# Kernel tuning notes

Hardware: AMD Instinct MI355X
Metric: run time of the kernel (lower is better)

## Reference

```python
import jax, jax.numpy as jnp
import numpy as np

B, T, D, K = 256, 256, 768, 128  # batch, seq_len, num_dims, num_state


def setup_inputs() -> dict:
    key = jax.random.key(0)
    k1, k2, k3 = jax.random.split(key, 3)
    s = jax.random.normal(k1, (B, T, D), dtype=jnp.float32)          # embeddings
    means = jax.random.normal(k2, (K, D), dtype=jnp.float32)         # per-state Gaussian means
    var = jax.random.uniform(k3, (D,), dtype=jnp.float32,
                             minval=0.5, maxval=1.5)                  # shared diagonal variance
    return {"s": s, "means": means, "var": var}


def reference(s, means, var):
    """DMVFlow._eval_log_density: per-state diagonal-Gaussian log density.

    density[b,t,k] = -0.5*(D*log(2*pi) + sum_d log var[d])
                     -0.5*sum_d (s[b,t,d] - means[k,d])^2 / var[d]
    Expanded quadratic form so the k-contraction is a single GEMM instead of
    materializing a (B,T,K,D) broadcast.
    """
    d = s.shape[-1]
    inv_var = 1.0 / var                                              # (D,)
    log_norm = -0.5 * (d * jnp.log(2.0 * jnp.pi) + jnp.sum(jnp.log(var)))
    s2 = jnp.einsum('btd,d->bt', s * s, inv_var)                     # (B,T)
    cross = jnp.einsum('btd,kd->btk', s, means * inv_var)            # (B,T,K) GEMM
    m2 = jnp.einsum('kd,d->k', means * means, inv_var)               # (K,)
    quad = s2[..., None] - 2.0 * cross + m2                          # (B,T,K)
    return log_norm - 0.5 * quad
```

## Files before the change

### kernel.cpp

```cpp
#include <hip/hip_runtime.h>
#include <stdint.h>

#define D_DIM    768
#define K_STATES 128
#define M_ROWS   65536
#define BM       64
#define BK       32
#define NSTEPS   (D_DIM / BK)
#define LDSTRIDE 40

typedef __attribute__((ext_vector_type(8))) short bf16x8;
typedef __attribute__((ext_vector_type(4))) float f32x4;
typedef __attribute__((ext_vector_type(4))) int   i32x4;

__device__ __forceinline__ unsigned short f2bf(float f) {
    union { float f; unsigned u; } x; x.f = f;
    unsigned r = (x.u + 0x7FFFu + ((x.u >> 16) & 1u)) >> 16;
    return (unsigned short)r;
}

__global__ void __launch_bounds__(256) prep_kernel(
        const float* __restrict__ means, const float* __restrict__ var,
        unsigned short* __restrict__ mwbf, float* __restrict__ cvec) {
    const int k = blockIdx.x;
    const int t = threadIdx.x;
    float m2 = 0.f, ld = 0.f;
    for (int d = t; d < D_DIM; d += 256) {
        float v  = var[d];
        float iv = 1.0f / v;
        float m  = means[k * D_DIM + d];
        mwbf[k * D_DIM + d] = f2bf(m * iv);
        m2 += m * m * iv;
        ld += logf(v);
    }
#pragma unroll
    for (int off = 32; off > 0; off >>= 1) {
        m2 += __shfl_down(m2, off, 64);
        ld += __shfl_down(ld, off, 64);
    }
    __shared__ float rm[4], rl[4];
    const int wid = t >> 6;
    if ((t & 63) == 0) { rm[wid] = m2; rl[wid] = ld; }
    __syncthreads();
    if (t == 0) {
        float M2 = rm[0] + rm[1] + rm[2] + rm[3];
        float LD = rl[0] + rl[1] + rl[2] + rl[3];
        cvec[k] = -0.5f * ((float)D_DIM * 1.8378770664093453f + LD + M2);
    }
}

__global__ void __launch_bounds__(256, 4) dmv_main(
        const float* __restrict__ s, const unsigned short* __restrict__ mwbf,
        const float* __restrict__ var, const float* __restrict__ cvec,
        float* __restrict__ out) {
    __shared__ unsigned short As[2][BM * LDSTRIDE];
    __shared__ unsigned short Bs[2][K_STATES * LDSTRIDE];
    __shared__ float ivs[D_DIM];
    __shared__ float part[BM][8];
    __shared__ float s2row[BM];
    __shared__ float cs[K_STATES];

    const int t    = threadIdx.x;
    const int lane = t & 63;
    const int w    = t >> 6;
    const int wr   = w >> 1;
    const int wc   = w & 1;
    const long rowBase = (long)blockIdx.x * BM;

    for (int d = t; d < D_DIM; d += 256) ivs[d] = 1.0f / var[d];
    if (t < K_STATES) cs[t] = cvec[t];

    const int arow0 = t >> 3;
    const int acol  = (t & 7) * 4;
    const int brow0 = t >> 2;
    const int bcol  = (t & 3) * 8;

    const float*          sA = s    + (rowBase + arow0) * D_DIM + acol;
    const unsigned short* sB = mwbf + brow0 * D_DIM + bcol;

    f32x4 aPref[2];
    i32x4 bPref[2];
    float s2acc[2] = {0.f, 0.f};

    f32x4 acc[2][4];
#pragma unroll
    for (int i = 0; i < 2; ++i)
#pragma unroll
        for (int j = 0; j < 4; ++j) acc[i][j] = f32x4{0.f, 0.f, 0.f, 0.f};

    auto stageWrite = [&](int buf, int k0) {
        f32x4 ivv = *reinterpret_cast<const f32x4*>(&ivs[k0 + acol]);
#pragma unroll
        for (int j = 0; j < 2; ++j) {
            const int row = j * 32 + arow0;
            f32x4 v = aPref[j];
            s2acc[j] += v[0]*v[0]*ivv[0] + v[1]*v[1]*ivv[1]
                      + v[2]*v[2]*ivv[2] + v[3]*v[3]*ivv[3];
            unsigned u0 = (unsigned)f2bf(v[0]) | ((unsigned)f2bf(v[1]) << 16);
            unsigned u1 = (unsigned)f2bf(v[2]) | ((unsigned)f2bf(v[3]) << 16);
            *reinterpret_cast<uint2*>(&As[buf][row * LDSTRIDE + acol]) = make_uint2(u0, u1);
        }
#pragma unroll
        for (int j = 0; j < 2; ++j) {
            const int row = j * 64 + brow0;
            *reinterpret_cast<i32x4*>(&Bs[buf][row * LDSTRIDE + bcol]) = bPref[j];
        }
    };

#pragma unroll
    for (int j = 0; j < 2; ++j) aPref[j] = *(const f32x4*)(sA + (long)j * 32 * D_DIM);
#pragma unroll
    for (int j = 0; j < 2; ++j) bPref[j] = *(const i32x4*)(sB + j * 64 * D_DIM);
    __syncthreads();
    stageWrite(0, 0);

    const int g  = (lane >> 4) * 8;
    const int rA = wr * 32 + (lane & 15);
    const int rB = wc * 64 + (lane & 15);

    for (int st = 0; st < NSTEPS; ++st) {
        const int cur = st & 1;
        const int k0n = (st + 1) * BK;
        if (st + 1 < NSTEPS) {
#pragma unroll
            for (int j = 0; j < 2; ++j)
                aPref[j] = *(const f32x4*)(sA + (long)j * 32 * D_DIM + k0n);
#pragma unroll
            for (int j = 0; j < 2; ++j)
                bPref[j] = *(const i32x4*)(sB + j * 64 * D_DIM + k0n);
        }
        __syncthreads();

        const unsigned short* Ab = &As[cur][0];
        const unsigned short* Bb = &Bs[cur][0];
        bf16x8 afrag[2], bfrag[4];
#pragma unroll
        for (int i = 0; i < 2; ++i)
            afrag[i] = *(const bf16x8*)(Ab + (rA + i * 16) * LDSTRIDE + g);
#pragma unroll
        for (int j = 0; j < 4; ++j)
            bfrag[j] = *(const bf16x8*)(Bb + (rB + j * 16) * LDSTRIDE + g);
#pragma unroll
        for (int i = 0; i < 2; ++i)
#pragma unroll
            for (int j = 0; j < 4; ++j)
                acc[i][j] = __builtin_amdgcn_mfma_f32_16x16x32_bf16(
                                afrag[i], bfrag[j], acc[i][j], 0, 0, 0);

        if (st + 1 < NSTEPS) stageWrite((st + 1) & 1, k0n);
    }

#pragma unroll
    for (int j = 0; j < 2; ++j) part[j * 32 + arow0][t & 7] = s2acc[j];
    __syncthreads();
    if (t < BM) {
        float v = 0.f;
#pragma unroll
        for (int sl = 0; sl < 8; ++sl) v += part[t][sl];
        s2row[t] = v;
    }
    __syncthreads();

    const int colBase = wc * 64 + (lane & 15);
#pragma unroll
    for (int i = 0; i < 2; ++i) {
        const int rl0 = wr * 32 + i * 16 + (lane >> 4) * 4;
#pragma unroll
        for (int j = 0; j < 4; ++j) {
            const int col = colBase + j * 16;
            const float cj = cs[col];
#pragma unroll
            for (int r = 0; r < 4; ++r) {
                const int rl = rl0 + r;
                out[(rowBase + rl) * K_STATES + col] = acc[i][j][r] + cj - 0.5f * s2row[rl];
            }
        }
    }
}

extern "C" void kernel_launch(void* const* d_in, const int* in_sizes, int n_in,
                              void* d_out, int out_size, void* d_ws, size_t ws_size,
                              hipStream_t stream) {
    const float* s     = (const float*)d_in[0];
    const float* means = (const float*)d_in[1];
    const float* var   = (const float*)d_in[2];
    float* out = (float*)d_out;

    unsigned short* mwbf = (unsigned short*)d_ws;
    float* cvec = (float*)((char*)d_ws + (size_t)K_STATES * D_DIM * sizeof(unsigned short));

    prep_kernel<<<K_STATES, 256, 0, stream>>>(means, var, mwbf, cvec);
    dmv_main<<<M_ROWS / BM, 256, 0, stream>>>(s, mwbf, var, cvec, out);
}
```

Before: 45.02 us.

## Fuse means/var preprocessing into main GEMM kernel and use nontemporal loads/stores

Removes the separate prep kernel. Each block of the main kernel now loads fp32 means directly, scales them by inverse variance, converts them to bf16 in LDS, and computes the per-state m2 and log-variance constants itself. The goal is to save one kernel launch and the workspace round trip. In exchange, every one of the 1024 blocks redoes the means scaling and bf16 conversion and fetches twice the B bytes (fp32 instead of bf16). The streaming s loads and output stores are also marked nontemporal, and the launch_bounds occupancy hint is dropped.

```diff
diff --git a/kernel.cpp b/kernel.cpp
--- a/kernel.cpp
+++ b/kernel.cpp
@@ -19,46 +19,16 @@
     return (unsigned short)r;
 }
 
-__global__ void __launch_bounds__(256) prep_kernel(
-        const float* __restrict__ means, const float* __restrict__ var,
-        unsigned short* __restrict__ mwbf, float* __restrict__ cvec) {
-    const int k = blockIdx.x;
-    const int t = threadIdx.x;
-    float m2 = 0.f, ld = 0.f;
-    for (int d = t; d < D_DIM; d += 256) {
-        float v  = var[d];
-        float iv = 1.0f / v;
-        float m  = means[k * D_DIM + d];
-        mwbf[k * D_DIM + d] = f2bf(m * iv);
-        m2 += m * m * iv;
-        ld += logf(v);
-    }
-#pragma unroll
-    for (int off = 32; off > 0; off >>= 1) {
-        m2 += __shfl_down(m2, off, 64);
-        ld += __shfl_down(ld, off, 64);
-    }
-    __shared__ float rm[4], rl[4];
-    const int wid = t >> 6;
-    if ((t & 63) == 0) { rm[wid] = m2; rl[wid] = ld; }
-    __syncthreads();
-    if (t == 0) {
-        float M2 = rm[0] + rm[1] + rm[2] + rm[3];
-        float LD = rl[0] + rl[1] + rl[2] + rl[3];
-        cvec[k] = -0.5f * ((float)D_DIM * 1.8378770664093453f + LD + M2);
-    }
-}
-
-__global__ void __launch_bounds__(256, 4) dmv_main(
-        const float* __restrict__ s, const unsigned short* __restrict__ mwbf,
-        const float* __restrict__ var, const float* __restrict__ cvec,
-        float* __restrict__ out) {
+__global__ void __launch_bounds__(256) dmv_fused(
+        const float* __restrict__ s, const float* __restrict__ means,
+        const float* __restrict__ var, float* __restrict__ out) {
     __shared__ unsigned short As[2][BM * LDSTRIDE];
     __shared__ unsigned short Bs[2][K_STATES * LDSTRIDE];
     __shared__ float ivs[D_DIM];
     __shared__ float part[BM][8];
     __shared__ float s2row[BM];
     __shared__ float cs[K_STATES];
+    __shared__ float rlg[4];
 
     const int t    = threadIdx.x;
     const int lane = t & 63;
@@ -67,20 +37,28 @@
     const int wc   = w & 1;
     const long rowBase = (long)blockIdx.x * BM;
 
-    for (int d = t; d < D_DIM; d += 256) ivs[d] = 1.0f / var[d];
-    if (t < K_STATES) cs[t] = cvec[t];
+    float ldp = 0.f;
+    for (int d = t; d < D_DIM; d += 256) {
+        float v = var[d];
+        ivs[d] = 1.0f / v;
+        ldp += logf(v);
+    }
+#pragma unroll
+    for (int off = 32; off > 0; off >>= 1) ldp += __shfl_down(ldp, off, 64);
+    if ((t & 63) == 0) rlg[t >> 6] = ldp;
 
     const int arow0 = t >> 3;
     const int acol  = (t & 7) * 4;
-    const int brow0 = t >> 2;
-    const int bcol  = (t & 3) * 8;
+    const int brow  = t >> 1;
+    const int bcol0 = (t & 1) * 16;
 
-    const float*          sA = s    + (rowBase + arow0) * D_DIM + acol;
-    const unsigned short* sB = mwbf + brow0 * D_DIM + bcol;
+    const float* sA = s     + (rowBase + arow0) * D_DIM + acol;
+    const float* sM = means + brow * D_DIM + bcol0;
 
     f32x4 aPref[2];
-    i32x4 bPref[2];
+    f32x4 bPref[4];
     float s2acc[2] = {0.f, 0.f};
+    float m2p = 0.f;
 
     f32x4 acc[2][4];
 #pragma unroll
@@ -100,18 +78,36 @@
             unsigned u1 = (unsigned)f2bf(v[2]) | ((unsigned)f2bf(v[3]) << 16);
             *reinterpret_cast<uint2*>(&As[buf][row * LDSTRIDE + acol]) = make_uint2(u0, u1);
         }
+        f32x4 mw[4];
 #pragma unroll
-        for (int j = 0; j < 2; ++j) {
-            const int row = j * 64 + brow0;
-            *reinterpret_cast<i32x4*>(&Bs[buf][row * LDSTRIDE + bcol]) = bPref[j];
+        for (int j = 0; j < 4; ++j) {
+            f32x4 iw = *reinterpret_cast<const f32x4*>(&ivs[k0 + bcol0 + j * 4]);
+            f32x4 mv = bPref[j];
+            m2p += mv[0]*mv[0]*iw[0] + mv[1]*mv[1]*iw[1]
+                 + mv[2]*mv[2]*iw[2] + mv[3]*mv[3]*iw[3];
+            mw[j] = f32x4{mv[0]*iw[0], mv[1]*iw[1], mv[2]*iw[2], mv[3]*iw[3]};
         }
+        i32x4 p0, p1;
+        p0.x = (int)((unsigned)f2bf(mw[0][0]) | ((unsigned)f2bf(mw[0][1]) << 16));
+        p0.y = (int)((unsigned)f2bf(mw[0][2]) | ((unsigned)f2bf(mw[0][3]) << 16));
+        p0.z = (int)((unsigned)f2bf(mw[1][0]) | ((unsigned)f2bf(mw[1][1]) << 16));
+        p0.w = (int)((unsigned)f2bf(mw[1][2]) | ((unsigned)f2bf(mw[1][3]) << 16));
+        p1.x = (int)((unsigned)f2bf(mw[2][0]) | ((unsigned)f2bf(mw[2][1]) << 16));
+        p1.y = (int)((unsigned)f2bf(mw[2][2]) | ((unsigned)f2bf(mw[2][3]) << 16));
+        p1.z = (int)((unsigned)f2bf(mw[3][0]) | ((unsigned)f2bf(mw[3][1]) << 16));
+        p1.w = (int)((unsigned)f2bf(mw[3][2]) | ((unsigned)f2bf(mw[3][3]) << 16));
+        *reinterpret_cast<i32x4*>(&Bs[buf][brow * LDSTRIDE + bcol0])     = p0;
+        *reinterpret_cast<i32x4*>(&Bs[buf][brow * LDSTRIDE + bcol0 + 8]) = p1;
     };
 
 #pragma unroll
-    for (int j = 0; j < 2; ++j) aPref[j] = *(const f32x4*)(sA + (long)j * 32 * D_DIM);
+    for (int j = 0; j < 2; ++j)
+        aPref[j] = __builtin_nontemporal_load((const f32x4*)(sA + (long)j * 32 * D_DIM));
 #pragma unroll
-    for (int j = 0; j < 2; ++j) bPref[j] = *(const i32x4*)(sB + j * 64 * D_DIM);
+    for (int j = 0; j < 4; ++j)
+        bPref[j] = *(const f32x4*)(sM + j * 4);
     __syncthreads();
+    const float slog = rlg[0] + rlg[1] + rlg[2] + rlg[3];
     stageWrite(0, 0);
 
     const int g  = (lane >> 4) * 8;
@@ -124,10 +120,11 @@
         if (st + 1 < NSTEPS) {
 #pragma unroll
             for (int j = 0; j < 2; ++j)
-                aPref[j] = *(const f32x4*)(sA + (long)j * 32 * D_DIM + k0n);
+                aPref[j] = __builtin_nontemporal_load(
+                               (const f32x4*)(sA + (long)j * 32 * D_DIM + k0n));
 #pragma unroll
-            for (int j = 0; j < 2; ++j)
-                bPref[j] = *(const i32x4*)(sB + j * 64 * D_DIM + k0n);
+            for (int j = 0; j < 4; ++j)
+                bPref[j] = *(const f32x4*)(sM + k0n + j * 4);
         }
         __syncthreads();
 
@@ -152,6 +149,11 @@
 
 #pragma unroll
     for (int j = 0; j < 2; ++j) part[j * 32 + arow0][t & 7] = s2acc[j];
+    {
+        float m2t = m2p + __shfl_xor(m2p, 1, 64);
+        if (!(t & 1))
+            cs[brow] = -0.5f * ((float)D_DIM * 1.8378770664093453f + slog + m2t);
+    }
     __syncthreads();
     if (t < BM) {
         float v = 0.f;
@@ -172,7 +174,8 @@
 #pragma unroll
             for (int r = 0; r < 4; ++r) {
                 const int rl = rl0 + r;
-                out[(rowBase + rl) * K_STATES + col] = acc[i][j][r] + cj - 0.5f * s2row[rl];
+                __builtin_nontemporal_store(acc[i][j][r] + cj - 0.5f * s2row[rl],
+                                            &out[(rowBase + rl) * K_STATES + col]);
             }
         }
     }
@@ -186,9 +189,5 @@
     const float* var   = (const float*)d_in[2];
     float* out = (float*)d_out;
 
-    unsigned short* mwbf = (unsigned short*)d_ws;
-    float* cvec = (float*)((char*)d_ws + (size_t)K_STATES * D_DIM * sizeof(unsigned short));
-
-    prep_kernel<<<K_STATES, 256, 0, stream>>>(means, var, mwbf, cvec);
-    dmv_main<<<M_ROWS / BM, 256, 0, stream>>>(s, mwbf, var, cvec, out);
+    dmv_fused<<<M_ROWS / BM, 256, 0, stream>>>(s, means, var, out);
 }
```

New measurement: 77.87 us. +73.0%, slower.

## Load GEMM operands directly into MFMA fragments, dropping LDS staging

Applied to the files above, without the earlier changes.

Removes the shared-memory double buffering of A and B tiles. Each wave now loads its own 32 rows of s and all 128 rows of the bf16 means straight from global memory into registers laid out as MFMA fragments, with a two-stage register prefetch. The block tile doubles to 128 rows and each wave holds all 128 output columns. The per-row s2 reduction now uses cross-lane shuffles instead of LDS, and outputs use nontemporal stores. The aim is to cut LDS traffic and barriers, at the cost of many more registers, lower occupancy, and every wave re-reading the B matrix from global memory or cache.

```diff
diff --git a/kernel.cpp b/kernel.cpp
--- a/kernel.cpp
+++ b/kernel.cpp
@@ -4,10 +4,9 @@
 #define D_DIM    768
 #define K_STATES 128
 #define M_ROWS   65536
-#define BM       64
+#define BM       128
 #define BK       32
 #define NSTEPS   (D_DIM / BK)
-#define LDSTRIDE 40
 
 typedef __attribute__((ext_vector_type(8))) short bf16x8;
 typedef __attribute__((ext_vector_type(4))) float f32x4;
@@ -49,133 +48,114 @@
     }
 }
 
-__global__ void __launch_bounds__(256, 4) dmv_main(
+__global__ void __launch_bounds__(256, 2) dmv_main(
         const float* __restrict__ s, const unsigned short* __restrict__ mwbf,
         const float* __restrict__ var, const float* __restrict__ cvec,
         float* __restrict__ out) {
-    __shared__ unsigned short As[2][BM * LDSTRIDE];
-    __shared__ unsigned short Bs[2][K_STATES * LDSTRIDE];
     __shared__ float ivs[D_DIM];
-    __shared__ float part[BM][8];
-    __shared__ float s2row[BM];
-    __shared__ float cs[K_STATES];
 
     const int t    = threadIdx.x;
     const int lane = t & 63;
     const int w    = t >> 6;
-    const int wr   = w >> 1;
-    const int wc   = w & 1;
-    const long rowBase = (long)blockIdx.x * BM;
+    const int r0   = lane & 15;
+    const int g    = (lane >> 4) * 8;
+    const long rowBase = (long)blockIdx.x * BM + w * 32;
 
-    for (int d = t; d < D_DIM; d += 256) ivs[d] = 1.0f / var[d];
-    if (t < K_STATES) cs[t] = cvec[t];
+    const float*          pA = s    + (rowBase + r0) * D_DIM + g;
+    const unsigned short* pB = mwbf + r0 * D_DIM + g;
 
-    const int arow0 = t >> 3;
-    const int acol  = (t & 7) * 4;
-    const int brow0 = t >> 2;
-    const int bcol  = (t & 3) * 8;
-
-    const float*          sA = s    + (rowBase + arow0) * D_DIM + acol;
-    const unsigned short* sB = mwbf + brow0 * D_DIM + bcol;
-
-    f32x4 aPref[2];
-    i32x4 bPref[2];
-    float s2acc[2] = {0.f, 0.f};
-
-    f32x4 acc[2][4];
+    f32x4 acc[2][8];
 #pragma unroll
     for (int i = 0; i < 2; ++i)
 #pragma unroll
-        for (int j = 0; j < 4; ++j) acc[i][j] = f32x4{0.f, 0.f, 0.f, 0.f};
+        for (int j = 0; j < 8; ++j) acc[i][j] = f32x4{0.f, 0.f, 0.f, 0.f};
 
-    auto stageWrite = [&](int buf, int k0) {
-        f32x4 ivv = *reinterpret_cast<const f32x4*>(&ivs[k0 + acol]);
-#pragma unroll
-        for (int j = 0; j < 2; ++j) {
-            const int row = j * 32 + arow0;
-            f32x4 v = aPref[j];
-            s2acc[j] += v[0]*v[0]*ivv[0] + v[1]*v[1]*ivv[1]
-                      + v[2]*v[2]*ivv[2] + v[3]*v[3]*ivv[3];
-            unsigned u0 = (unsigned)f2bf(v[0]) | ((unsigned)f2bf(v[1]) << 16);
-            unsigned u1 = (unsigned)f2bf(v[2]) | ((unsigned)f2bf(v[3]) << 16);
-            *reinterpret_cast<uint2*>(&As[buf][row * LDSTRIDE + acol]) = make_uint2(u0, u1);
-        }
-#pragma unroll
-        for (int j = 0; j < 2; ++j) {
-            const int row = j * 64 + brow0;
-            *reinterpret_cast<i32x4*>(&Bs[buf][row * LDSTRIDE + bcol]) = bPref[j];
-        }
-    };
+    f32x4 a0_[2][2], a1_[2][2];
+    i32x4 b0_[8], b1_[8];
 
-#pragma unroll
-    for (int j = 0; j < 2; ++j) aPref[j] = *(const f32x4*)(sA + (long)j * 32 * D_DIM);
-#pragma unroll
-    for (int j = 0; j < 2; ++j) bPref[j] = *(const i32x4*)(sB + j * 64 * D_DIM);
+#define LOADA(DST, ST) do {                                                    \
+    _Pragma("unroll")                                                          \
+    for (int i = 0; i < 2; ++i) {                                              \
+        const float* p = pA + (long)i * 16 * D_DIM + (ST) * BK;                \
+        DST[i][0] = *(const f32x4*)(p);                                        \
+        DST[i][1] = *(const f32x4*)(p + 4);                                    \
+    } } while (0)
+
+#define LOADB(DST, ST) do {                                                    \
+    _Pragma("unroll")                                                          \
+    for (int j = 0; j < 8; ++j)                                                \
+        DST[j] = *(const i32x4*)(pB + (long)j * 16 * D_DIM + (ST) * BK);       \
+    } while (0)
+
+    LOADA(a0_, 0); LOADB(b0_, 0);
+    LOADA(a1_, 1); LOADB(b1_, 1);
+
+    for (int d = t; d < D_DIM; d += 256) ivs[d] = 1.0f / var[d];
     __syncthreads();
-    stageWrite(0, 0);
 
-    const int g  = (lane >> 4) * 8;
-    const int rA = wr * 32 + (lane & 15);
-    const int rB = wc * 64 + (lane & 15);
+    float s2acc[2] = {0.f, 0.f};
 
-    for (int st = 0; st < NSTEPS; ++st) {
-        const int cur = st & 1;
-        const int k0n = (st + 1) * BK;
-        if (st + 1 < NSTEPS) {
-#pragma unroll
-            for (int j = 0; j < 2; ++j)
-                aPref[j] = *(const f32x4*)(sA + (long)j * 32 * D_DIM + k0n);
-#pragma unroll
-            for (int j = 0; j < 2; ++j)
-                bPref[j] = *(const i32x4*)(sB + j * 64 * D_DIM + k0n);
-        }
-        __syncthreads();
+#define STEP(ARAW, BRAW, K0) do {                                              \
+    f32x4 iv0 = *(const f32x4*)&ivs[(K0) + g];                                 \
+    f32x4 iv1 = *(const f32x4*)&ivs[(K0) + g + 4];                             \
+    bf16x8 af[2];                                                              \
+    _Pragma("unroll")                                                          \
+    for (int i = 0; i < 2; ++i) {                                              \
+        f32x4 v0 = ARAW[i][0], v1 = ARAW[i][1];                                \
+        s2acc[i] += v0[0]*v0[0]*iv0[0] + v0[1]*v0[1]*iv0[1]                    \
+                  + v0[2]*v0[2]*iv0[2] + v0[3]*v0[3]*iv0[3]                    \
+                  + v1[0]*v1[0]*iv1[0] + v1[1]*v1[1]*iv1[1]                    \
+                  + v1[2]*v1[2]*iv1[2] + v1[3]*v1[3]*iv1[3];                   \
+        union { bf16x8 h; unsigned u[4]; } pk;                                 \
+        pk.u[0] = (unsigned)f2bf(v0[0]) | ((unsigned)f2bf(v0[1]) << 16);       \
+        pk.u[1] = (unsigned)f2bf(v0[2]) | ((unsigned)f2bf(v0[3]) << 16);       \
+        pk.u[2] = (unsigned)f2bf(v1[0]) | ((unsigned)f2bf(v1[1]) << 16);       \
+        pk.u[3] = (unsigned)f2bf(v1[2]) | ((unsigned)f2bf(v1[3]) << 16);       \
+        af[i] = pk.h;                                                          \
+    }                                                                          \
+    _Pragma("unroll")                                                          \
+    for (int j = 0; j < 8; ++j) {                                              \
+        union { i32x4 i; bf16x8 h; } bb; bb.i = BRAW[j];                       \
+        acc[0][j] = __builtin_amdgcn_mfma_f32_16x16x32_bf16(af[0], bb.h,       \
+                                                            acc[0][j], 0,0,0);\
+        acc[1][j] = __builtin_amdgcn_mfma_f32_16x16x32_bf16(af[1], bb.h,       \
+                                                            acc[1][j], 0,0,0);\
+    } } while (0)
 
-        const unsigned short* Ab = &As[cur][0];
-        const unsigned short* Bb = &Bs[cur][0];
-        bf16x8 afrag[2], bfrag[4];
-#pragma unroll
-        for (int i = 0; i < 2; ++i)
-            afrag[i] = *(const bf16x8*)(Ab + (rA + i * 16) * LDSTRIDE + g);
-#pragma unroll
-        for (int j = 0; j < 4; ++j)
-            bfrag[j] = *(const bf16x8*)(Bb + (rB + j * 16) * LDSTRIDE + g);
-#pragma unroll
-        for (int i = 0; i < 2; ++i)
-#pragma unroll
-            for (int j = 0; j < 4; ++j)
-                acc[i][j] = __builtin_amdgcn_mfma_f32_16x16x32_bf16(
-                                afrag[i], bfrag[j], acc[i][j], 0, 0, 0);
-
-        if (st + 1 < NSTEPS) stageWrite((st + 1) & 1, k0n);
+    for (int st = 0; st < NSTEPS; st += 2) {
+        STEP(a0_, b0_, st * BK);
+        if (st + 2 < NSTEPS) { LOADA(a0_, st + 2); LOADB(b0_, st + 2); }
+        STEP(a1_, b1_, (st + 1) * BK);
+        if (st + 3 < NSTEPS) { LOADA(a1_, st + 3); LOADB(b1_, st + 3); }
     }
 
 #pragma unroll
-    for (int j = 0; j < 2; ++j) part[j * 32 + arow0][t & 7] = s2acc[j];
-    __syncthreads();
-    if (t < BM) {
-        float v = 0.f;
+    for (int i = 0; i < 2; ++i) {
+        s2acc[i] += __shfl_xor(s2acc[i], 16, 64);
+        s2acc[i] += __shfl_xor(s2acc[i], 32, 64);
+    }
+
+    float cj[8];
 #pragma unroll
-        for (int sl = 0; sl < 8; ++sl) v += part[t][sl];
-        s2row[t] = v;
-    }
-    __syncthreads();
+    for (int j = 0; j < 8; ++j) cj[j] = cvec[j * 16 + r0];
 
-    const int colBase = wc * 64 + (lane & 15);
+    const int q = lane >> 4;
 #pragma unroll
     for (int i = 0; i < 2; ++i) {
-        const int rl0 = wr * 32 + i * 16 + (lane >> 4) * 4;
 #pragma unroll
-        for (int j = 0; j < 4; ++j) {
-            const int col = colBase + j * 16;
-            const float cj = cs[col];
+        for (int r = 0; r < 4; ++r) {
+            float s2v = __shfl(s2acc[i], q * 4 + r, 64);
+            const long row = rowBase + i * 16 + q * 4 + r;
+            float* po = out + row * K_STATES + r0;
+            const float base = -0.5f * s2v;
 #pragma unroll
-            for (int r = 0; r < 4; ++r) {
-                const int rl = rl0 + r;
-                out[(rowBase + rl) * K_STATES + col] = acc[i][j][r] + cj - 0.5f * s2row[rl];
-            }
+            for (int j = 0; j < 8; ++j)
+                __builtin_nontemporal_store(acc[i][j][r] + cj[j] + base, po + j * 16);
         }
     }
+#undef LOADA
+#undef LOADB
+#undef STEP
 }
 
 extern "C" void kernel_launch(void* const* d_in, const int* in_sizes, int n_in,
```

Result: slower. 79.23 us (+76.0%).

## Deepen global prefetch to two register stages and unroll K loop by two

Applied to the files above, without the earlier changes.

Holds two register prefetch sets so global loads for step st+2/st+3 are issued two iterations ahead, and unrolls the K loop by two with fixed LDS buffer indices. It also swaps the manual bf16 rounding for the HIP __float22bfloat162_rn packed conversion. The aim is to hide more global-memory latency and cut index and select overhead. In exchange it uses more registers, which could hurt the 4-blocks-per-CU occupancy target.

```diff
diff --git a/kernel.cpp b/kernel.cpp
--- a/kernel.cpp
+++ b/kernel.cpp
@@ -1,4 +1,5 @@
 #include <hip/hip_runtime.h>
+#include <hip/hip_bf16.h>
 #include <stdint.h>
 
 #define D_DIM    768
@@ -78,8 +79,8 @@
     const float*          sA = s    + (rowBase + arow0) * D_DIM + acol;
     const unsigned short* sB = mwbf + brow0 * D_DIM + bcol;
 
-    f32x4 aPref[2];
-    i32x4 bPref[2];
+    f32x4 a0_[2], a1_[2];
+    i32x4 b0_[2], b1_[2];
     float s2acc[2] = {0.f, 0.f};
 
     f32x4 acc[2][4];
@@ -88,66 +89,72 @@
 #pragma unroll
         for (int j = 0; j < 4; ++j) acc[i][j] = f32x4{0.f, 0.f, 0.f, 0.f};
 
-    auto stageWrite = [&](int buf, int k0) {
-        f32x4 ivv = *reinterpret_cast<const f32x4*>(&ivs[k0 + acol]);
-#pragma unroll
-        for (int j = 0; j < 2; ++j) {
-            const int row = j * 32 + arow0;
-            f32x4 v = aPref[j];
-            s2acc[j] += v[0]*v[0]*ivv[0] + v[1]*v[1]*ivv[1]
-                      + v[2]*v[2]*ivv[2] + v[3]*v[3]*ivv[3];
-            unsigned u0 = (unsigned)f2bf(v[0]) | ((unsigned)f2bf(v[1]) << 16);
-            unsigned u1 = (unsigned)f2bf(v[2]) | ((unsigned)f2bf(v[3]) << 16);
-            *reinterpret_cast<uint2*>(&As[buf][row * LDSTRIDE + acol]) = make_uint2(u0, u1);
-        }
-#pragma unroll
-        for (int j = 0; j < 2; ++j) {
-            const int row = j * 64 + brow0;
-            *reinterpret_cast<i32x4*>(&Bs[buf][row * LDSTRIDE + bcol]) = bPref[j];
-        }
-    };
-
-#pragma unroll
-    for (int j = 0; j < 2; ++j) aPref[j] = *(const f32x4*)(sA + (long)j * 32 * D_DIM);
-#pragma unroll
-    for (int j = 0; j < 2; ++j) bPref[j] = *(const i32x4*)(sB + j * 64 * D_DIM);
-    __syncthreads();
-    stageWrite(0, 0);
+#define LOADP(AP, BP, ST) do {                                                 \
+    AP[0] = *(const f32x4*)(sA + (ST) * BK);                                   \
+    AP[1] = *(const f32x4*)(sA + (long)32 * D_DIM + (ST) * BK);                \
+    BP[0] = *(const i32x4*)(sB + (ST) * BK);                                   \
+    BP[1] = *(const i32x4*)(sB + (long)64 * D_DIM + (ST) * BK);                \
+} while (0)
+
+#define STAGE(BUF, AP, BP, K0) do {                                            \
+    f32x4 ivv = *reinterpret_cast<const f32x4*>(&ivs[(K0) + acol]);            \
+    _Pragma("unroll")                                                          \
+    for (int j = 0; j < 2; ++j) {                                              \
+        const int row = j * 32 + arow0;                                        \
+        f32x4 v = AP[j];                                                       \
+        s2acc[j] += v[0]*v[0]*ivv[0] + v[1]*v[1]*ivv[1]                        \
+                  + v[2]*v[2]*ivv[2] + v[3]*v[3]*ivv[3];                       \
+        __hip_bfloat162 p0 = __float22bfloat162_rn(make_float2(v[0], v[1]));   \
+        __hip_bfloat162 p1 = __float22bfloat162_rn(make_float2(v[2], v[3]));   \
+        union { uint2 u2; __hip_bfloat162 h[2]; } pk;                          \
+        pk.h[0] = p0; pk.h[1] = p1;                                            \
+        *reinterpret_cast<uint2*>(&As[BUF][row * LDSTRIDE + acol]) = pk.u2;    \
+    }                                                                          \
+    _Pragma("unroll")                                                          \
+    for (int j = 0; j < 2; ++j)                                                \
+        *reinterpret_cast<i32x4*>(&Bs[BUF][(j * 64 + brow0) * LDSTRIDE + bcol])\
+            = BP[j];                                                           \
+} while (0)
 
     const int g  = (lane >> 4) * 8;
     const int rA = wr * 32 + (lane & 15);
     const int rB = wc * 64 + (lane & 15);
 
-    for (int st = 0; st < NSTEPS; ++st) {
-        const int cur = st & 1;
-        const int k0n = (st + 1) * BK;
-        if (st + 1 < NSTEPS) {
-#pragma unroll
-            for (int j = 0; j < 2; ++j)
-                aPref[j] = *(const f32x4*)(sA + (long)j * 32 * D_DIM + k0n);
-#pragma unroll
-            for (int j = 0; j < 2; ++j)
-                bPref[j] = *(const i32x4*)(sB + j * 64 * D_DIM + k0n);
-        }
+#define COMPUTE(BUF) do {                                                      \
+    const unsigned short* Ab = &As[BUF][0];                                    \
+    const unsigned short* Bb = &Bs[BUF][0];                                    \
+    bf16x8 afrag[2], bfrag[4];                                                 \
+    _Pragma("unroll")                                                          \
+    for (int i = 0; i < 2; ++i)                                                \
+        afrag[i] = *(const bf16x8*)(Ab + (rA + i * 16) * LDSTRIDE + g);        \
+    _Pragma("unroll")                                                          \
+    for (int j = 0; j < 4; ++j)                                                \
+        bfrag[j] = *(const bf16x8*)(Bb + (rB + j * 16) * LDSTRIDE + g);        \
+    _Pragma("unroll")                                                          \
+    for (int i = 0; i < 2; ++i)                                                \
+        _Pragma("unroll")                                                      \
+        for (int j = 0; j < 4; ++j)                                            \
+            acc[i][j] = __builtin_amdgcn_mfma_f32_16x16x32_bf16(               \
+                            afrag[i], bfrag[j], acc[i][j], 0, 0, 0);           \
+} while (0)
+
+    LOADP(a0_, b0_, 0);
+    LOADP(a1_, b1_, 1);
+    __syncthreads();
+    STAGE(0, a0_, b0_, 0);
+    LOADP(a0_, b0_, 2);
+    __syncthreads();
+
+    for (int st = 0; st < NSTEPS; st += 2) {
+        COMPUTE(0);
+        STAGE(1, a1_, b1_, (st + 1) * BK);
+        if (st + 3 < NSTEPS) LOADP(a1_, b1_, st + 3);
         __syncthreads();
 
-        const unsigned short* Ab = &As[cur][0];
-        const unsigned short* Bb = &Bs[cur][0];
-        bf16x8 afrag[2], bfrag[4];
-#pragma unroll
-        for (int i = 0; i < 2; ++i)
-            afrag[i] = *(const bf16x8*)(Ab + (rA + i * 16) * LDSTRIDE + g);
-#pragma unroll
-        for (int j = 0; j < 4; ++j)
-            bfrag[j] = *(const bf16x8*)(Bb + (rB + j * 16) * LDSTRIDE + g);
-#pragma unroll
-        for (int i = 0; i < 2; ++i)
-#pragma unroll
-            for (int j = 0; j < 4; ++j)
-                acc[i][j] = __builtin_amdgcn_mfma_f32_16x16x32_bf16(
-                                afrag[i], bfrag[j], acc[i][j], 0, 0, 0);
-
-        if (st + 1 < NSTEPS) stageWrite((st + 1) & 1, k0n);
+        COMPUTE(1);
+        if (st + 2 < NSTEPS) STAGE(0, a0_, b0_, (st + 2) * BK);
+        if (st + 4 < NSTEPS) LOADP(a0_, b0_, st + 4);
+        __syncthreads();
     }
 
 #pragma unroll
@@ -176,6 +183,9 @@
             }
         }
     }
+#undef LOADP
+#undef STAGE
+#undef COMPUTE
 }
 
 extern "C" void kernel_launch(void* const* d_in, const int* in_sizes, int n_in,
```

After: 46.02 us. 1.02x slower.
